# Optimization experiments

Hardware: AMD Instinct MI355X
Metric: run time of the kernel (lower is better)

## Reference

```python
import jax, jax.numpy as jnp
import numpy as np

HIDDEN = 2304
HEADS = 16
THETA = 10000.0
LN_EPS = 1e-5


def setup_inputs() -> dict:
    key = jax.random.key(0)
    ks = jax.random.split(key, 6)
    d = HIDDEN
    init = lambda k, shape: jax.random.normal(k, shape, jnp.float32) * 0.02
    return {
        "x": jax.random.normal(ks[0], (4, 2048, d), jnp.float32),
        "wq": init(ks[1], (d, d)), "bq": jnp.zeros((d,), jnp.float32),
        "wk": init(ks[2], (d, d)), "bk": jnp.zeros((d,), jnp.float32),
        "wv": init(ks[3], (d, d)), "bv": jnp.zeros((d,), jnp.float32),
        "wo": init(ks[4], (d, d)), "bo": jnp.zeros((d,), jnp.float32),
        "ln_g": jnp.ones((d,), jnp.float32),
        "ln_b": jnp.zeros((d,), jnp.float32),
    }


def reference(x, wq, bq, wk, bk, wv, bv, wo, bo, ln_g, ln_b):
    b, s, d = x.shape
    H = HEADS
    Dh = d // H

    # qkv projections (nn.Linear: x @ W^T + b)
    q = jnp.einsum('bsd,ed->bse', x, wq) + bq
    k = jnp.einsum('bsd,ed->bse', x, wk) + bk
    v = jnp.einsum('bsd,ed->bse', x, wv) + bv

    # RoPE over the FULL hidden dim (d/2 pairs), as in the source
    pos = jnp.arange(s, dtype=jnp.float32)                    # (s,)
    scale = jnp.arange(0, d, 2, dtype=jnp.float32) / d        # (d/2,)
    omega = 1.0 / (THETA ** scale)                            # (d/2,)
    ang = pos[:, None] * omega[None, :]                       # (s, d/2)
    cos, sin = jnp.cos(ang), jnp.sin(ang)

    def rot(t):
        t2 = t.reshape(b, s, d // 2, 2)
        x0, x1 = t2[..., 0], t2[..., 1]
        return jnp.stack([cos * x0 - sin * x1, sin * x0 + cos * x1], axis=-1).reshape(b, s, d)

    q, k = rot(q), rot(k)

    # split heads -> (b, H, s, Dh)
    q = q.reshape(b, s, H, Dh).transpose(0, 2, 1, 3)
    k = k.reshape(b, s, H, Dh).transpose(0, 2, 1, 3)
    v = v.reshape(b, s, H, Dh).transpose(0, 2, 1, 3)

    # NOTE: faithful to source: einsum labels make this HEAD-mixing
    # attention at each position: logits shape (b, H, s, H)
    att_scale = 1.0 / (Dh ** 0.5)
    logits = jnp.einsum('bnhd,bmhd->bnhm', q, k) * att_scale
    w = jax.nn.softmax(logits, axis=-1)                       # (b,H,s,H)
    out = jnp.einsum('bnhm,bmhd->bnhd', w, v)                 # (b,H,s,Dh)

    out = out.transpose(0, 2, 1, 3).reshape(b, s, d)
    out = jnp.einsum('bsd,ed->bse', out, wo) + bo

    # residual + LayerNorm (dropout in eval mode -> identity)
    y = x + out
    mu = jnp.mean(y, axis=-1, keepdims=True)
    var = jnp.mean((y - mu) ** 2, axis=-1, keepdims=True)
    return (y - mu) * jax.lax.rsqrt(var + LN_EPS) * ln_g + ln_b
```

## Files before the change

### kernel.cpp

```cpp
#include <hip/hip_runtime.h>
#include <stdint.h>
#include <stddef.h>

#define D_HID 2304
#define NTOK  8192
#define NQKV  6912
#define WELEMS 5308416
#define SEQ_MASK 2047

typedef unsigned short u16;
typedef __bf16 bf16x8 __attribute__((ext_vector_type(8)));
typedef float  f32x16 __attribute__((ext_vector_type(16)));

__device__ __forceinline__ u16 f2bf(float f) {
    unsigned int u = __builtin_bit_cast(unsigned int, f);
    u += 0x7fffu + ((u >> 16) & 1u);
    return (u16)(u >> 16);
}
__device__ __forceinline__ float bf2f(u16 h) {
    unsigned int u = ((unsigned int)h) << 16;
    return __builtin_bit_cast(float, u);
}

__device__ __forceinline__ void gl2lds16(const void* g, void* l) {
    __builtin_amdgcn_global_load_lds(
        (const __attribute__((address_space(1))) void*)g,
        (__attribute__((address_space(3))) void*)l,
        16, 0, 0);
}

__global__ __launch_bounds__(256) void cvt_f32_bf16(
    const float* __restrict__ src, u16* __restrict__ dst)
{
    size_t i = ((size_t)blockIdx.x * 256 + threadIdx.x) * 4;
    float4 f = *(const float4*)(src + i);
    ushort4 o = make_ushort4(f2bf(f.x), f2bf(f.y), f2bf(f.z), f2bf(f.w));
    *(ushort4*)(dst + i) = o;
}

__global__ __launch_bounds__(256) void cvt_weights(
    const float* __restrict__ wq, const float* __restrict__ wk,
    const float* __restrict__ wv, const float* __restrict__ wo,
    u16* __restrict__ dst,
    const float* __restrict__ bq, const float* __restrict__ bk,
    const float* __restrict__ bv, float* __restrict__ bqkv)
{
    int i = blockIdx.x * 256 + threadIdx.x;
    if (i < NQKV)
        bqkv[i] = (i < 2304) ? bq[i] : (i < 4608) ? bk[i - 2304] : bv[i - 4608];
    size_t base = (size_t)i * 4;
    int r = (int)(base / WELEMS);
    const float* src = (r == 0) ? wq : (r == 1) ? wk : (r == 2) ? wv : wo;
    float4 f = *(const float4*)(src + (base - (size_t)r * WELEMS));
    ushort4 o = make_ushort4(f2bf(f.x), f2bf(f.y), f2bf(f.z), f2bf(f.w));
    *(ushort4*)(dst + base) = o;
}

template<int MODE>
__global__ __launch_bounds__(256, 3) void gemm_bt(
    const u16* __restrict__ A, const u16* __restrict__ B,
    const float* __restrict__ bias, u16* __restrict__ Cout,
    const u16* __restrict__ resid, int M, int N, int K)
{
    __shared__ __align__(16) u16 As[128 * 64];
    __shared__ __align__(16) u16 Bs[128 * 64];

    const int tid  = threadIdx.x;
    const int lane = tid & 63;
    const int wave = tid >> 6;

    const int num_bn = N >> 7;
    const int rem = blockIdx.x % (num_bn << 3);
    const int bn  = rem >> 3;
    const int bm  = ((blockIdx.x / (num_bn << 3)) << 3) + (rem & 7);

    const int srow = tid >> 3;
    const int sc   = (tid & 7) ^ (srow & 7);
    const u16* Ag = A + (size_t)(bm * 128 + srow) * K + sc * 8;
    const u16* Bg = B + (size_t)(bn * 128 + srow) * K + sc * 8;
    const size_t row32 = (size_t)32 * K;
    u16* asd = As + wave * 512;
    u16* bsd = Bs + wave * 512;

    const int rl = lane & 31;
    const int h  = lane >> 5;
    const int swz = rl & 7;
    const int wm = (wave >> 1) * 64;
    const int wn = (wave & 1) * 64;

    f32x16 acc[2][2] = {};

    for (int kb = 0; kb < K; kb += 64) {
        __syncthreads();
#pragma unroll
        for (int r = 0; r < 4; ++r) {
            gl2lds16(Ag + kb + r * row32, asd + r * 2048);
            gl2lds16(Bg + kb + r * row32, bsd + r * 2048);
        }
        __syncthreads();

#pragma unroll
        for (int s = 0; s < 4; ++s) {
            const int ch = ((s * 2 + h) ^ swz) * 8;
            bf16x8 a0 = *(const bf16x8*)(As + (wm      + rl) * 64 + ch);
            bf16x8 a1 = *(const bf16x8*)(As + (wm + 32 + rl) * 64 + ch);
            bf16x8 b0 = *(const bf16x8*)(Bs + (wn      + rl) * 64 + ch);
            bf16x8 b1 = *(const bf16x8*)(Bs + (wn + 32 + rl) * 64 + ch);
            acc[0][0] = __builtin_amdgcn_mfma_f32_32x32x16_bf16(a0, b0, acc[0][0], 0, 0, 0);
            acc[0][1] = __builtin_amdgcn_mfma_f32_32x32x16_bf16(a0, b1, acc[0][1], 0, 0, 0);
            acc[1][0] = __builtin_amdgcn_mfma_f32_32x32x16_bf16(a1, b0, acc[1][0], 0, 0, 0);
            acc[1][1] = __builtin_amdgcn_mfma_f32_32x32x16_bf16(a1, b1, acc[1][1], 0, 0, 0);
        }
    }

#pragma unroll
    for (int mt = 0; mt < 2; ++mt) {
#pragma unroll
        for (int nt = 0; nt < 2; ++nt) {
            const int gn = bn * 128 + wn + nt * 32 + rl;
            const float bv = bias[gn];
#pragma unroll
            for (int reg = 0; reg < 16; ++reg) {
                const int gm = bm * 128 + wm + mt * 32 +
                               (reg & 3) + 8 * (reg >> 2) + 4 * h;
                const size_t idx = (size_t)gm * N + gn;
                float v = acc[mt][nt][reg] + bv;
                if constexpr (MODE == 1) v += bf2f(resid[idx]);
                Cout[idx] = f2bf(v);
            }
        }
    }
}

#define HROW 148
__global__ __launch_bounds__(256) void attn_headmix(
    const u16* __restrict__ QKV, u16* __restrict__ Aout)
{
    __shared__ __align__(16) float qs[16 * HROW];
    __shared__ __align__(16) float ks[16 * HROW];
    __shared__ __align__(16) float vs[16 * HROW];
    __shared__ __align__(16) float wsmT[256];

    const int tid = threadIdx.x;
    const int t   = blockIdx.x;
    const float fpos = (float)(t & SEQ_MASK);
    const u16* row = QKV + (size_t)t * NQKV;

    const float OMEGA_C = -2.0f * 13.287712379549449f / 2304.0f;
    const float INV2PI  = 0.15915494309189535f;

    for (int c = tid; c < 864; c += 256) {
        uint4 raw = *(const uint4*)(row + c * 8);
        float f[8];
        f[0] = bf2f(raw.x & 0xffff); f[1] = bf2f(raw.x >> 16);
        f[2] = bf2f(raw.y & 0xffff); f[3] = bf2f(raw.y >> 16);
        f[4] = bf2f(raw.z & 0xffff); f[5] = bf2f(raw.z >> 16);
        f[6] = bf2f(raw.w & 0xffff); f[7] = bf2f(raw.w >> 16);
        if (c < 576) {
            const int cc = (c < 288) ? c : c - 288;
            const int p0 = cc * 4;
#pragma unroll
            for (int jp = 0; jp < 4; ++jp) {
                float omega = exp2f((float)(p0 + jp) * OMEGA_C);
                float rr = fpos * omega * INV2PI;
                rr -= floorf(rr);
                float sn = __builtin_amdgcn_sinf(rr);
                float cs = __builtin_amdgcn_cosf(rr);
                float x0 = f[2 * jp], x1 = f[2 * jp + 1];
                f[2 * jp]     = cs * x0 - sn * x1;
                f[2 * jp + 1] = sn * x0 + cs * x1;
            }
            const int hr = cc / 18, col = (cc - hr * 18) * 8;
            float* dst = ((c < 288) ? qs : ks) + hr * HROW + col;
            *(float4*)(dst)     = make_float4(f[0], f[1], f[2], f[3]);
            *(float4*)(dst + 4) = make_float4(f[4], f[5], f[6], f[7]);
        } else {
            const int cv = c - 576;
            const int hr = cv / 18, col = (cv - hr * 18) * 8;
            float* dst = vs + hr * HROW + col;
            *(float4*)(dst)     = make_float4(f[0], f[1], f[2], f[3]);
            *(float4*)(dst + 4) = make_float4(f[4], f[5], f[6], f[7]);
        }
    }
    __syncthreads();

    const int n = tid >> 4, m = tid & 15;
    const float* qr = qs + n * HROW;
    const float* kr = ks + m * HROW;
    float s = 0.f;
#pragma unroll
    for (int d = 0; d < 144; d += 4) {
        float4 qv = *(const float4*)(qr + d);
        float4 kv = *(const float4*)(kr + d);
        s += qv.x * kv.x + qv.y * kv.y + qv.z * kv.z + qv.w * kv.w;
    }
    s *= (1.0f / 12.0f);

    float mx = s;
#pragma unroll
    for (int off = 8; off >= 1; off >>= 1) mx = fmaxf(mx, __shfl_xor(mx, off));
    float e = __expf(s - mx);
    float sum = e;
#pragma unroll
    for (int off = 8; off >= 1; off >>= 1) sum += __shfl_xor(sum, off);
    wsmT[m * 16 + n] = e / sum;
    __syncthreads();

    if (tid < 144) {
        const int col4 = tid % 36;
        const int nq   = tid / 36;
        const int oc   = col4 * 4;
        float4 a0 = {0,0,0,0}, a1 = {0,0,0,0}, a2 = {0,0,0,0}, a3 = {0,0,0,0};
#pragma unroll
        for (int mm = 0; mm < 16; ++mm) {
            float4 w4 = *(const float4*)(wsmT + mm * 16 + nq * 4);
            float4 v4 = *(const float4*)(vs + mm * HROW + oc);
            a0.x += w4.x * v4.x; a0.y += w4.x * v4.y; a0.z += w4.x * v4.z; a0.w += w4.x * v4.w;
            a1.x += w4.y * v4.x; a1.y += w4.y * v4.y; a1.z += w4.y * v4.z; a1.w += w4.y * v4.w;
            a2.x += w4.z * v4.x; a2.y += w4.z * v4.y; a2.z += w4.z * v4.z; a2.w += w4.z * v4.w;
            a3.x += w4.w * v4.x; a3.y += w4.w * v4.y; a3.z += w4.w * v4.z; a3.w += w4.w * v4.w;
        }
        u16* orow = Aout + (size_t)t * D_HID;
        float4 accs[4] = {a0, a1, a2, a3};
#pragma unroll
        for (int i = 0; i < 4; ++i) {
            const int nn = nq * 4 + i;
            ushort4 o = make_ushort4(f2bf(accs[i].x), f2bf(accs[i].y),
                                     f2bf(accs[i].z), f2bf(accs[i].w));
            *(ushort4*)(orow + nn * 144 + oc) = o;
        }
    }
}

__global__ __launch_bounds__(256) void ln_kernel(
    const u16* __restrict__ Y, const float* __restrict__ g,
    const float* __restrict__ b, float* __restrict__ out)
{
    const int tid  = threadIdx.x;
    const u16* y = Y + (size_t)blockIdx.x * D_HID;
    float v[9];
    float s = 0.f, s2 = 0.f;
#pragma unroll
    for (int r = 0; r < 9; ++r) {
        v[r] = bf2f(y[tid + r * 256]);
        s += v[r]; s2 += v[r] * v[r];
    }
#pragma unroll
    for (int off = 32; off >= 1; off >>= 1) {
        s  += __shfl_xor(s, off);
        s2 += __shfl_xor(s2, off);
    }
    __shared__ float red[8];
    const int wave = tid >> 6;
    if ((tid & 63) == 0) { red[wave] = s; red[4 + wave] = s2; }
    __syncthreads();
    s  = red[0] + red[1] + red[2] + red[3];
    s2 = red[4] + red[5] + red[6] + red[7];
    const float inv_n = 1.0f / 2304.0f;
    float mu  = s * inv_n;
    float var = fmaxf(s2 * inv_n - mu * mu, 0.f);
    float inv = rsqrtf(var + 1e-5f);
    float* orow = out + (size_t)blockIdx.x * D_HID;
#pragma unroll
    for (int r = 0; r < 9; ++r) {
        int c = tid + r * 256;
        orow[c] = (v[r] - mu) * inv * g[c] + b[c];
    }
}

extern "C" void kernel_launch(void* const* d_in, const int* in_sizes, int n_in,
                              void* d_out, int out_size, void* d_ws, size_t ws_size,
                              hipStream_t stream)
{
    const float* x   = (const float*)d_in[0];
    const float* wq  = (const float*)d_in[1];
    const float* bq  = (const float*)d_in[2];
    const float* wk  = (const float*)d_in[3];
    const float* bk  = (const float*)d_in[4];
    const float* wv  = (const float*)d_in[5];
    const float* bv  = (const float*)d_in[6];
    const float* wo  = (const float*)d_in[7];
    const float* bo  = (const float*)d_in[8];
    const float* lng = (const float*)d_in[9];
    const float* lnb = (const float*)d_in[10];

    char* ws = (char*)d_ws;
    size_t off = 0;
    auto alloc = [&](size_t bytes) {
        void* p = ws + off;
        off += (bytes + 255) & ~(size_t)255;
        return p;
    };
    u16*   xb   = (u16*)alloc((size_t)NTOK * D_HID * 2);
    u16*   wqkv = (u16*)alloc((size_t)(NQKV + D_HID) * D_HID * 2);
    u16*   wob  = wqkv + (size_t)NQKV * D_HID;
    float* bqkv = (float*)alloc((size_t)NQKV * 4);
    u16*   qkv  = (u16*)alloc((size_t)NTOK * NQKV * 2);
    u16*   aout = (u16*)alloc((size_t)NTOK * D_HID * 2);
    u16*   ybuf = qkv;

    cvt_f32_bf16<<<NTOK * D_HID / 1024, 256, 0, stream>>>(x, xb);
    cvt_weights<<<4 * WELEMS / 1024, 256, 0, stream>>>(wq, wk, wv, wo, wqkv,
                                                       bq, bk, bv, bqkv);
    gemm_bt<0><<<(NQKV / 128) * (NTOK / 128), 256, 0, stream>>>(
        xb, wqkv, bqkv, qkv, nullptr, NTOK, NQKV, D_HID);
    attn_headmix<<<NTOK, 256, 0, stream>>>(qkv, aout);
    gemm_bt<1><<<(D_HID / 128) * (NTOK / 128), 256, 0, stream>>>(
        aout, wob, bo, ybuf, xb, NTOK, D_HID, D_HID);
    ln_kernel<<<NTOK, 256, 0, stream>>>(ybuf, lng, lnb, (float*)d_out);
}
```

Baseline: 692.7 us.

## Add 256x256-tile 8-wave GEMM with staged LDS pipeline for QKV projection

Replaces the 128x128 QKV projection GEMM with a new 512-thread kernel that computes 256x256 output tiles. It uses 16x16x32 bf16 MFMA, a double-buffered 128KB LDS with XOR swizzle, and global-to-LDS loads split into quarter-tile stages interleaved with compute phases. It also adds XCD-aware block remapping and s_setprio around MFMA bursts. The larger tile raises operand reuse and cuts global traffic, at the cost of one block per CU from LDS limits, heavy register pressure, and uncoalesced scalar bf16 stores in the epilogue.

Result: faster. 660.8 us (-4.6%).

```diff
diff --git a/kernel.cpp b/kernel.cpp
--- a/kernel.cpp
+++ b/kernel.cpp
@@ -11,6 +11,7 @@
 typedef unsigned short u16;
 typedef __bf16 bf16x8 __attribute__((ext_vector_type(8)));
 typedef float  f32x16 __attribute__((ext_vector_type(16)));
+typedef float  f32x4  __attribute__((ext_vector_type(4)));
 
 __device__ __forceinline__ u16 f2bf(float f) {
     unsigned int u = __builtin_bit_cast(unsigned int, f);
@@ -54,6 +55,164 @@
     float4 f = *(const float4*)(src + (base - (size_t)r * WELEMS));
     ushort4 o = make_ushort4(f2bf(f.x), f2bf(f.y), f2bf(f.z), f2bf(f.w));
     *(ushort4*)(dst + base) = o;
+}
+
+__global__ __launch_bounds__(512, 2) void gemm256_bt(
+    const u16* __restrict__ A, const u16* __restrict__ B,
+    const float* __restrict__ bias, u16* __restrict__ Cout,
+    int M, int N, int K)
+{
+    __shared__ __align__(16) u16 lds2[65536];
+
+    const int tid  = threadIdx.x;
+    const int lane = tid & 63;
+    const int wave = tid >> 6;
+    const int NT   = K >> 6;
+    (void)M;
+
+    const int chunk = gridDim.x >> 3;
+    const int bid = (blockIdx.x & 7) * chunk + (blockIdx.x >> 3);
+    const int num_bn = N >> 8;
+    const int bm = bid / num_bn;
+    const int bn = bid - bm * num_bn;
+
+    const int srow = lane >> 3;
+    const u16* __restrict__ Ast = A + (size_t)(bm * 256 + wave * 8 + srow) * K
+                                    + ((lane & 7) ^ srow) * 8;
+    const u16* __restrict__ Bst = B + (size_t)(bn * 256 + wave * 8 + srow) * K
+                                    + ((lane & 7) ^ srow) * 8;
+    const size_t row64  = (size_t)64 * K;
+    const size_t row128 = (size_t)128 * K;
+    const int ldsW = wave * 512;
+
+#define STAGE(buf, hsel, tt) do {                                              \
+    const u16* g_ = ((hsel) < 2 ? Ast : Bst)                                   \
+                    + (((hsel) & 1) ? row128 : 0) + (size_t)(tt) * 64;         \
+    u16* l_ = lds2 + (buf) * 32768 + (((hsel) < 2) ? 0 : 16384)                \
+              + (((hsel) & 1) ? 8192 : 0) + ldsW;                              \
+    gl2lds16(g_, l_);                                                          \
+    gl2lds16(g_ + row64, l_ + 4096);                                           \
+} while (0)
+
+    const int l15 = lane & 15, l4 = lane >> 4;
+    const int aBase = (wave >> 2) * 8192 + l15 * 64;
+    const int bBase = 16384 + ((wave >> 1) & 1) * 8192
+                      + ((wave & 1) * 64 + l15) * 64;
+    const int s0 = ((l4    ) ^ (lane & 7)) * 8;
+    const int s1 = ((l4 + 4) ^ (lane & 7)) * 8;
+
+    f32x4 acc[8][4] = {};
+
+    STAGE(0, 2, 0); STAGE(0, 3, 0); STAGE(0, 0, 0); STAGE(0, 1, 0);
+    STAGE(1, 2, 1); STAGE(1, 3, 1); STAGE(1, 0, 1);
+    asm volatile("s_waitcnt vmcnt(6)" ::: "memory");
+    __builtin_amdgcn_s_barrier();
+
+    for (int t = 0; t < NT; ++t) {
+        const int cur = t & 1;
+        const u16* lc = lds2 + cur * 32768;
+        const bool stg2 = (t + 2 < NT);
+        bf16x8 bfr[4][2], am[2][2], ah[4][2];
+
+#pragma unroll
+        for (int n = 0; n < 4; ++n) {
+            bfr[n][0] = *(const bf16x8*)(lc + bBase + n * 1024 + s0);
+            bfr[n][1] = *(const bf16x8*)(lc + bBase + n * 1024 + s1);
+        }
+#pragma unroll
+        for (int mo = 0; mo < 2; ++mo) {
+            am[mo][0] = *(const bf16x8*)(lc + aBase + mo * 1024 + s0);
+            am[mo][1] = *(const bf16x8*)(lc + aBase + mo * 1024 + s1);
+        }
+        if (t + 1 < NT) STAGE(cur ^ 1, 1, t + 1);
+        __builtin_amdgcn_s_barrier();
+        asm volatile("s_waitcnt lgkmcnt(0)" ::: "memory");
+        __builtin_amdgcn_sched_barrier(0);
+        __builtin_amdgcn_s_setprio(1);
+#pragma unroll
+        for (int kk = 0; kk < 2; ++kk)
+#pragma unroll
+            for (int mo = 0; mo < 2; ++mo)
+#pragma unroll
+                for (int n = 0; n < 4; ++n)
+                    acc[mo][n] = __builtin_amdgcn_mfma_f32_16x16x32_bf16(
+                        am[mo][kk], bfr[n][kk], acc[mo][n], 0, 0, 0);
+        __builtin_amdgcn_s_setprio(0);
+        __builtin_amdgcn_s_barrier();
+
+#pragma unroll
+        for (int mo = 0; mo < 2; ++mo) {
+            am[mo][0] = *(const bf16x8*)(lc + aBase + (2 + mo) * 1024 + s0);
+            am[mo][1] = *(const bf16x8*)(lc + aBase + (2 + mo) * 1024 + s1);
+        }
+        if (stg2) STAGE(cur, 2, t + 2);
+        __builtin_amdgcn_s_barrier();
+        asm volatile("s_waitcnt lgkmcnt(0)" ::: "memory");
+        __builtin_amdgcn_sched_barrier(0);
+        __builtin_amdgcn_s_setprio(1);
+#pragma unroll
+        for (int kk = 0; kk < 2; ++kk)
+#pragma unroll
+            for (int mo = 0; mo < 2; ++mo)
+#pragma unroll
+                for (int n = 0; n < 4; ++n)
+                    acc[2 + mo][n] = __builtin_amdgcn_mfma_f32_16x16x32_bf16(
+                        am[mo][kk], bfr[n][kk], acc[2 + mo][n], 0, 0, 0);
+        __builtin_amdgcn_s_setprio(0);
+        __builtin_amdgcn_s_barrier();
+
+#pragma unroll
+        for (int mo = 0; mo < 4; ++mo) {
+            ah[mo][0] = *(const bf16x8*)(lc + aBase + (4 + mo) * 1024 + s0);
+            ah[mo][1] = *(const bf16x8*)(lc + aBase + (4 + mo) * 1024 + s1);
+        }
+        if (stg2) STAGE(cur, 3, t + 2);
+        __builtin_amdgcn_s_barrier();
+        asm volatile("s_waitcnt lgkmcnt(0)" ::: "memory");
+        __builtin_amdgcn_sched_barrier(0);
+        __builtin_amdgcn_s_setprio(1);
+#pragma unroll
+        for (int kk = 0; kk < 2; ++kk)
+#pragma unroll
+            for (int mo = 0; mo < 2; ++mo)
+#pragma unroll
+                for (int n = 0; n < 4; ++n)
+                    acc[4 + mo][n] = __builtin_amdgcn_mfma_f32_16x16x32_bf16(
+                        ah[mo][kk], bfr[n][kk], acc[4 + mo][n], 0, 0, 0);
+        __builtin_amdgcn_s_setprio(0);
+        __builtin_amdgcn_s_barrier();
+
+        if (stg2) STAGE(cur, 0, t + 2);
+        __builtin_amdgcn_s_barrier();
+        __builtin_amdgcn_s_setprio(1);
+#pragma unroll
+        for (int kk = 0; kk < 2; ++kk)
+#pragma unroll
+            for (int mo = 0; mo < 2; ++mo)
+#pragma unroll
+                for (int n = 0; n < 4; ++n)
+                    acc[6 + mo][n] = __builtin_amdgcn_mfma_f32_16x16x32_bf16(
+                        ah[2 + mo][kk], bfr[n][kk], acc[6 + mo][n], 0, 0, 0);
+        __builtin_amdgcn_s_setprio(0);
+        if (t < NT - 2)       asm volatile("s_waitcnt vmcnt(6)" ::: "memory");
+        else if (t == NT - 2) asm volatile("s_waitcnt vmcnt(0)" ::: "memory");
+        __builtin_amdgcn_s_barrier();
+    }
+#undef STAGE
+
+    const int wm0 = (wave >> 2) * 128, wn0 = (wave & 3) * 64;
+#pragma unroll
+    for (int n = 0; n < 4; ++n) {
+        const int gn = bn * 256 + wn0 + n * 16 + l15;
+        const float bv = bias[gn];
+#pragma unroll
+        for (int m = 0; m < 8; ++m) {
+            const int gm = bm * 256 + wm0 + m * 16 + l4 * 4;
+#pragma unroll
+            for (int j = 0; j < 4; ++j)
+                Cout[(size_t)(gm + j) * N + gn] = f2bf(acc[m][n][j] + bv);
+        }
+    }
 }
 
 template<int MODE>
@@ -302,8 +461,8 @@
     cvt_f32_bf16<<<NTOK * D_HID / 1024, 256, 0, stream>>>(x, xb);
     cvt_weights<<<4 * WELEMS / 1024, 256, 0, stream>>>(wq, wk, wv, wo, wqkv,
                                                        bq, bk, bv, bqkv);
-    gemm_bt<0><<<(NQKV / 128) * (NTOK / 128), 256, 0, stream>>>(
-        xb, wqkv, bqkv, qkv, nullptr, NTOK, NQKV, D_HID);
+    gemm256_bt<<<(NTOK / 256) * (NQKV / 256), 512, 0, stream>>>(
+        xb, wqkv, bqkv, qkv, NTOK, NQKV, D_HID);
     attn_headmix<<<NTOK, 256, 0, stream>>>(qkv, aout);
     gemm_bt<1><<<(D_HID / 128) * (NTOK / 128), 256, 0, stream>>>(
         aout, wob, bo, ybuf, xb, NTOK, D_HID, D_HID);
```
